# Performance work log

Hardware: AMD Instinct MI355X
Metric: run time of the kernel (lower is better)

## Reference

```python
import jax, jax.numpy as jnp
import numpy as np

NUM_CLASSES = 80
B, P = 16, 22743  # batch, total anchors (3 * (76^2 + 38^2 + 19^2))


def _bce(p, t):
    # torch.nn.BCELoss math with log clamped at -100 (torch's internal clamp)
    logp = jnp.maximum(jnp.log(p), -100.0)
    log1mp = jnp.maximum(jnp.log1p(-p), -100.0)
    return -(t * logp + (1.0 - t) * log1mp)


def setup_inputs() -> dict:
    key = jax.random.key(0)
    k = jax.random.split(key, 7)
    eps = 1e-4  # keep sigmoid outputs strictly inside (0,1)
    add_sigmoid = jax.random.uniform(k[0], (B, P, 5 + NUM_CLASSES), jnp.float32, eps, 1.0 - eps)
    loc_t = jax.random.uniform(k[1], (B, P, 4), jnp.float32)
    conf_t = jax.random.uniform(k[2], (B, P), jnp.float32)
    scale_t = jax.random.uniform(k[3], (B, P), jnp.float32, 0.0, 2.0)
    cls_t = jax.random.randint(k[4], (B, P), 0, NUM_CLASSES, jnp.int32)
    fore_mask = jax.random.bernoulli(k[5], 0.02, (B, P))
    back_mask = jnp.logical_not(fore_mask)
    return {"add_sigmoid": add_sigmoid, "loc_t": loc_t, "conf_t": conf_t,
            "scale_t": scale_t, "cls_t": cls_t, "fore_mask": fore_mask,
            "back_mask": back_mask}


def reference(add_sigmoid, loc_t, conf_t, scale_t, cls_t, fore_mask, back_mask):
    batch = add_sigmoid.shape[0]
    dt = add_sigmoid.dtype
    fore = fore_mask.astype(dt)
    back = back_mask.astype(dt)

    # ---- classification loss: BCE(cls_pred[fore], one_hot(cls_t[fore])), sum-reduced
    cls_pred = add_sigmoid[..., 5:]                      # [B,P,C]
    one_hot = jax.nn.one_hot(cls_t, NUM_CLASSES, dtype=dt)
    cls_loss = jnp.sum(fore[..., None] * _bce(cls_pred, one_hot)) / batch

    # ---- confidence loss: fore-BCE + back-BCE, sum-reduced
    conf_pred = add_sigmoid[..., 4]                      # [B,P]
    conf_bce = _bce(conf_pred, conf_t)
    conf_loss = jnp.sum((fore + back) * conf_bce) / batch

    # ---- localization loss: scale-weighted MSE (WeightMseLoss, size_average=False)
    loc_pred = add_sigmoid[..., :4]                      # [B,P,4]
    diff2 = jnp.square(loc_t - loc_pred)
    w = (fore * scale_t)[..., None]                      # [B,P,1]
    xy_loss = jnp.sum(w * diff2[..., :2]) / 2.0
    wh_loss = jnp.sum(w * diff2[..., 2:]) / 2.0
    loc_loss = (xy_loss + wh_loss) / batch

    return loc_loss + conf_loss + cls_loss
```

## Files before the change

kernel.cpp:

```cpp
#include <hip/hip_runtime.h>

#define CH 85
#define BATCH 16
#define BLOCK 1024
#define FBLOCK 256

__global__ void __launch_bounds__(BLOCK)
multibox_main(const float* __restrict__ add_sigmoid,
              const float* __restrict__ loc_t,
              const float* __restrict__ conf_t,
              const float* __restrict__ scale_t,
              const int*   __restrict__ cls_t,
              const unsigned char* __restrict__ fore_m,
              const unsigned char* __restrict__ back_m,
              float* __restrict__ partials,
              int n)
{
    const bool is_u8 =
        (((fore_m[1] ^ back_m[1]) | (fore_m[2] ^ back_m[2]) | (fore_m[3] ^ back_m[3])) & 1) != 0;
    const int* fore_i32 = (const int*)fore_m;

    const int i         = blockIdx.x * BLOCK + threadIdx.x;
    const int lane      = threadIdx.x & 63;
    const int wave_base = blockIdx.x * BLOCK + (threadIdx.x & ~63);

    float acc = 0.f;
    bool fore_b = false;
    if (i < n) {
        fore_b = is_u8 ? (fore_m[i] != 0) : (fore_i32[i] != 0);
        const float cp  = add_sigmoid[(size_t)i * CH + 4];
        const float t   = conf_t[i];
        const float lp  = __logf(cp);
        const float l1p = __logf(1.f - cp);
        acc = -__builtin_fmaf(t, lp - l1p, l1p);
    }

    unsigned long long m = __ballot(fore_b);
    while (m) {
        const int src = (int)__ffsll((long long)m) - 1;
        m &= m - 1;
        const int a = wave_base + src;
        const float* base = add_sigmoid + (size_t)a * CH;
        const int k = cls_t[a];

        float c = 0.f;
        const float p = base[lane];
        if (lane < 4) {
            const float d = loc_t[4 * (size_t)a + lane] - p;
            c = scale_t[a] * 0.5f * d * d;
        } else if (lane >= 5) {
            c = (lane - 5 == k) ? -__logf(p) : -__logf(1.f - p);
        }
        if (lane < CH - 64) {
            const float p2 = base[lane + 64];
            c += (lane + 59 == k) ? -__logf(p2) : -__logf(1.f - p2);
        }
        acc += c;
    }

    #pragma unroll
    for (int off = 32; off > 0; off >>= 1)
        acc += __shfl_down(acc, off, 64);
    __shared__ float wsum[BLOCK / 64];
    const int wid = threadIdx.x >> 6;
    if (lane == 0) wsum[wid] = acc;
    __syncthreads();
    if (threadIdx.x == 0) {
        float s = 0.f;
        #pragma unroll
        for (int w = 0; w < BLOCK / 64; ++w) s += wsum[w];
        partials[blockIdx.x] = s;
    }
}

__global__ void __launch_bounds__(FBLOCK)
multibox_finalize(const float* __restrict__ partials, float* __restrict__ out, int g)
{
    float acc = 0.f;
    for (int j = threadIdx.x; j < g; j += FBLOCK) acc += partials[j];
    #pragma unroll
    for (int off = 32; off > 0; off >>= 1)
        acc += __shfl_down(acc, off, 64);
    __shared__ float wsum[FBLOCK / 64];
    const int lane = threadIdx.x & 63, wid = threadIdx.x >> 6;
    if (lane == 0) wsum[wid] = acc;
    __syncthreads();
    if (threadIdx.x == 0)
        out[0] = (wsum[0] + wsum[1] + wsum[2] + wsum[3]) * (1.f / BATCH);
}

extern "C" void kernel_launch(void* const* d_in, const int* in_sizes, int n_in,
                              void* d_out, int out_size, void* d_ws, size_t ws_size,
                              hipStream_t stream) {
    const float* add_sigmoid = (const float*)d_in[0];
    const float* loc_t       = (const float*)d_in[1];
    const float* conf_t      = (const float*)d_in[2];
    const float* scale_t     = (const float*)d_in[3];
    const int*   cls_t       = (const int*)d_in[4];
    const unsigned char* fore_m = (const unsigned char*)d_in[5];
    const unsigned char* back_m = (const unsigned char*)d_in[6];
    float* out = (float*)d_out;

    const int n    = in_sizes[2];
    const int grid = (n + BLOCK - 1) / BLOCK;

    float* partials = (float*)d_ws;

    multibox_main<<<grid, BLOCK, 0, stream>>>(
        add_sigmoid, loc_t, conf_t, scale_t, cls_t, fore_m, back_m, partials, n);
    multibox_finalize<<<1, FBLOCK, 0, stream>>>(partials, out, grid);
}
```

Baseline: 19.92 us.

## Stage add_sigmoid rows through LDS with coalesced float4 loads

Each block now copies a contiguous tile of 192 rows of add_sigmoid into shared memory with vectorized float4 loads, then reads confidence and foreground class/loc values from LDS. Previously the conf column was a strided 4-byte gather and foreground rows were read directly from global memory. The tradeoff is that the whole tensor is now streamed, including class columns of background rows that were never needed, along with about 65 KB of LDS per block and smaller 256-thread blocks. With only about 2% foreground, this makes the kernel fully bandwidth-bound on the full 85-channel tensor.

```diff
diff --git a/kernel.cpp b/kernel.cpp
--- a/kernel.cpp
+++ b/kernel.cpp
@@ -2,7 +2,9 @@
 
 #define CH 85
 #define BATCH 16
-#define BLOCK 1024
+#define BLOCK 256
+#define ROWS 192
+#define F4_PER_BLOCK (ROWS * CH / 4)
 #define FBLOCK 256
 
 __global__ void __launch_bounds__(BLOCK)
@@ -16,19 +18,37 @@
               float* __restrict__ partials,
               int n)
 {
+    __shared__ float lds[ROWS * CH];
+    __shared__ float wsum[BLOCK / 64];
+
     const bool is_u8 =
         (((fore_m[1] ^ back_m[1]) | (fore_m[2] ^ back_m[2]) | (fore_m[3] ^ back_m[3])) & 1) != 0;
     const int* fore_i32 = (const int*)fore_m;
 
-    const int i         = blockIdx.x * BLOCK + threadIdx.x;
-    const int lane      = threadIdx.x & 63;
-    const int wave_base = blockIdx.x * BLOCK + (threadIdx.x & ~63);
+    const int lane = threadIdx.x & 63;
+    const int wid  = threadIdx.x >> 6;
+    const int r0   = blockIdx.x * ROWS;
 
+    {
+        const float4* src = (const float4*)add_sigmoid;
+        float4* dst = (float4*)lds;
+        const long long total_f4 = (long long)n * CH / 4;
+        const long long f4_base  = (long long)blockIdx.x * F4_PER_BLOCK;
+        #pragma unroll
+        for (int k = threadIdx.x; k < F4_PER_BLOCK; k += BLOCK) {
+            const long long g = f4_base + k;
+            if (g < total_f4) dst[k] = src[g];
+        }
+    }
+    __syncthreads();
+
+    const int r = threadIdx.x;
+    const int i = r0 + r;
     float acc = 0.f;
     bool fore_b = false;
-    if (i < n) {
+    if (r < ROWS && i < n) {
         fore_b = is_u8 ? (fore_m[i] != 0) : (fore_i32[i] != 0);
-        const float cp  = add_sigmoid[(size_t)i * CH + 4];
+        const float cp  = lds[CH * r + 4];
         const float t   = conf_t[i];
         const float lp  = __logf(cp);
         const float l1p = __logf(1.f - cp);
@@ -36,15 +56,16 @@
     }
 
     unsigned long long m = __ballot(fore_b);
+    const int wave_row0 = wid * 64;
     while (m) {
         const int src = (int)__ffsll((long long)m) - 1;
         m &= m - 1;
-        const int a = wave_base + src;
-        const float* base = add_sigmoid + (size_t)a * CH;
-        const int k = cls_t[a];
+        const int ar = wave_row0 + src;
+        const int a  = r0 + ar;
+        const int k  = cls_t[a];
 
         float c = 0.f;
-        const float p = base[lane];
+        const float p = lds[CH * ar + lane];
         if (lane < 4) {
             const float d = loc_t[4 * (size_t)a + lane] - p;
             c = scale_t[a] * 0.5f * d * d;
@@ -52,7 +73,7 @@
             c = (lane - 5 == k) ? -__logf(p) : -__logf(1.f - p);
         }
         if (lane < CH - 64) {
-            const float p2 = base[lane + 64];
+            const float p2 = lds[CH * ar + 64 + lane];
             c += (lane + 59 == k) ? -__logf(p2) : -__logf(1.f - p2);
         }
         acc += c;
@@ -61,16 +82,10 @@
     #pragma unroll
     for (int off = 32; off > 0; off >>= 1)
         acc += __shfl_down(acc, off, 64);
-    __shared__ float wsum[BLOCK / 64];
-    const int wid = threadIdx.x >> 6;
     if (lane == 0) wsum[wid] = acc;
     __syncthreads();
-    if (threadIdx.x == 0) {
-        float s = 0.f;
-        #pragma unroll
-        for (int w = 0; w < BLOCK / 64; ++w) s += wsum[w];
-        partials[blockIdx.x] = s;
-    }
+    if (threadIdx.x == 0)
+        partials[blockIdx.x] = wsum[0] + wsum[1] + wsum[2] + wsum[3];
 }
 
 __global__ void __launch_bounds__(FBLOCK)
@@ -102,7 +117,7 @@
     float* out = (float*)d_out;
 
     const int n    = in_sizes[2];
-    const int grid = (n + BLOCK - 1) / BLOCK;
+    const int grid = (n + ROWS - 1) / ROWS;
 
     float* partials = (float*)d_ws;
 
```

Result: slower. 45.52 us (+128.5%).
